# Kernel optimization log

Hardware: AMD Instinct MI355X
Metric: run time of the kernel (lower is better)

## Reference

```python
import jax, jax.numpy as jnp
import numpy as np
from jax import lax

B, DIM, DIM_OUT, NH = 8, 512, 512, 8
HD = DIM_OUT // NH          # 64, also the depthwise-conv channel count
SQ, SKV = (1, 1), (2, 2)    # stride_q, stride_kv
PAD = 1                      # kernel 3 -> padding 3//2
SCALE = HD ** -0.5
EPS = 1e-6


def _dw_conv(x, w, stride):
    # x: [N, C, H, W], w: [C, 1, kh, kw]; depthwise conv (groups = C), no bias
    return lax.conv_general_dilated(
        x, w, window_strides=stride, padding=[(PAD, PAD), (PAD, PAD)],
        dimension_numbers=('NCHW', 'OIHW', 'NCHW'),
        feature_group_count=x.shape[1])


def _ln(x, w, b):
    m = jnp.mean(x, -1, keepdims=True)
    v = jnp.var(x, -1, keepdims=True)
    return (x - m) * lax.rsqrt(v + EPS) * w + b


def _pool(t, w, stride, ln_w, ln_b, H, W):
    # t: [B, NH, 1+H*W, HD] with cls token at index 0
    Bn = t.shape[0]
    cls = t[:, :, :1, :]
    body = t[:, :, 1:, :].reshape(Bn * NH, H, W, HD).transpose(0, 3, 1, 2)
    body = _dw_conv(body, w, stride)
    ph, pw = body.shape[2], body.shape[3]
    body = body.reshape(Bn, NH, HD, ph * pw).transpose(0, 1, 3, 2)
    out = jnp.concatenate([cls, body], axis=2)
    return _ln(out, ln_w, ln_b), (ph, pw)


def _rel_bias(r_q4, q_shape, k_shape, rel_pos_h, rel_pos_w):
    # r_q4: [B, NH, q_h*q_w, HD] (cls token stripped)
    q_h, q_w = q_shape
    k_h, k_w = k_shape

    def dist(qs, ks):
        qr, kr = max(ks / qs, 1.0), max(qs / ks, 1.0)
        d = np.arange(qs)[:, None] * qr - np.arange(ks)[None, :] * kr + (ks - 1) * kr
        return d.astype(np.int64)

    Rh = rel_pos_h[dist(q_h, k_h)]  # [q_h, k_h, HD]
    Rw = rel_pos_w[dist(q_w, k_w)]  # [q_w, k_w, HD]
    r_q = r_q4.reshape(r_q4.shape[0], NH, q_h, q_w, HD)
    rel_h = jnp.einsum('byhwc,hkc->byhwk', r_q, Rh)  # [B,NH,q_h,q_w,k_h]
    rel_w = jnp.einsum('byhwc,wkc->byhwk', r_q, Rw)  # [B,NH,q_h,q_w,k_w]
    return rel_h[..., :, None] + rel_w[..., None, :]  # [B,NH,q_h,q_w,k_h,k_w]


def setup_inputs() -> dict:
    key = jax.random.key(0)
    ks = jax.random.split(key, 16)
    H = W = 56
    N = H * W + 1
    rel_dim = 2 * H - 1  # 111
    return {
        'x': jax.random.normal(ks[0], (B, N, DIM), jnp.float32),
        'qkv_w': jax.random.normal(ks[1], (3 * DIM_OUT, DIM), jnp.float32) * DIM ** -0.5,
        'qkv_b': jax.random.normal(ks[2], (3 * DIM_OUT,), jnp.float32) * 0.02,
        'proj_w': jax.random.normal(ks[3], (DIM_OUT, DIM_OUT), jnp.float32) * DIM_OUT ** -0.5,
        'proj_b': jax.random.normal(ks[4], (DIM_OUT,), jnp.float32) * 0.02,
        'pool_q_w': jax.random.normal(ks[5], (HD, 1, 3, 3), jnp.float32) / 3.0,
        'pool_k_w': jax.random.normal(ks[6], (HD, 1, 3, 3), jnp.float32) / 3.0,
        'pool_v_w': jax.random.normal(ks[7], (HD, 1, 3, 3), jnp.float32) / 3.0,
        'lnq_w': 1.0 + 0.1 * jax.random.normal(ks[8], (HD,), jnp.float32),
        'lnq_b': 0.02 * jax.random.normal(ks[9], (HD,), jnp.float32),
        'lnk_w': 1.0 + 0.1 * jax.random.normal(ks[10], (HD,), jnp.float32),
        'lnk_b': 0.02 * jax.random.normal(ks[11], (HD,), jnp.float32),
        'lnv_w': 1.0 + 0.1 * jax.random.normal(ks[12], (HD,), jnp.float32),
        'lnv_b': 0.02 * jax.random.normal(ks[13], (HD,), jnp.float32),
        'rel_pos_h': 0.02 * jax.random.normal(ks[14], (rel_dim, HD), jnp.float32),
        'rel_pos_w': 0.02 * jax.random.normal(ks[15], (rel_dim, HD), jnp.float32),
        'hw_h': 56,
        'hw_w': 56,
    }


def reference(x, qkv_w, qkv_b, proj_w, proj_b, pool_q_w, pool_k_w, pool_v_w,
              lnq_w, lnq_b, lnk_w, lnk_b, lnv_w, lnv_b, rel_pos_h, rel_pos_w,
              hw_h, hw_w):
    Bn, N, _ = x.shape
    qkv = (x @ qkv_w.T + qkv_b).reshape(Bn, N, 3, NH, HD).transpose(2, 0, 3, 1, 4)
    q, k, v = qkv[0], qkv[1], qkv[2]  # each [B, NH, N, HD]
    q, q_shape = _pool(q, pool_q_w, SQ, lnq_w, lnq_b, hw_h, hw_w)
    k, k_shape = _pool(k, pool_k_w, SKV, lnk_w, lnk_b, hw_h, hw_w)
    v, _ = _pool(v, pool_v_w, SKV, lnv_w, lnv_b, hw_h, hw_w)
    attn = (q * SCALE) @ k.swapaxes(-2, -1)  # [B, NH, Nq, Nk]
    q_h, q_w = q_shape
    k_h, k_w = k_shape
    bias = _rel_bias(q[:, :, 1:, :], q_shape, k_shape, rel_pos_h, rel_pos_w)
    blk = attn[:, :, 1:, 1:].reshape(Bn, NH, q_h, q_w, k_h, k_w) + bias
    attn = attn.at[:, :, 1:, 1:].set(blk.reshape(Bn, NH, q_h * q_w, k_h * k_w))
    attn = jax.nn.softmax(attn, axis=-1)
    out = attn @ v                                   # [B, NH, Nq, HD]
    out = out.at[:, :, 1:, :].add(q[:, :, 1:, :])    # residual on non-cls rows
    out = out.transpose(0, 2, 1, 3).reshape(Bn, -1, DIM_OUT)
    return out @ proj_w.T + proj_b
```

## Files before the change

### kernel.cpp

```cpp
#include <hip/hip_runtime.h>
#include <hip/hip_bf16.h>
#include <cstdint>
#include <cstddef>

#define BB 8
#define NHH 8
#define NQ 3137
#define NKV 785
#define HDIM 64
#define MROWS (BB*NQ)
#define SCALE 0.125f
#define VTP 832

typedef unsigned short ushort_t;
typedef __attribute__((ext_vector_type(8))) short s16x8;
typedef __attribute__((ext_vector_type(4))) float f32x4;
typedef __attribute__((ext_vector_type(16))) float f32x16;

__device__ __forceinline__ float bf2f(ushort_t u) {
  union { unsigned int i; float f; } v; v.i = ((unsigned int)u) << 16; return v.f;
}
__device__ __forceinline__ ushort_t f2bf(float f) {
  union { float f; unsigned int i; } v; v.f = f;
  unsigned int r = v.i + 0x7fffu + ((v.i >> 16) & 1u);
  return (ushort_t)(r >> 16);
}
__device__ __forceinline__ unsigned int cvt_pk_bf16(float lo, float hi) {
  unsigned int r;
  asm("v_cvt_pk_bf16_f32 %0, %1, %2" : "=v"(r) : "v"(lo), "v"(hi));
  return r;
}
__device__ __forceinline__ s16x8 lds_frag(const ushort_t* base, int row, int slot) {
  const char* p = (const char*)base + row * 128 + (((slot ^ (row & 7)) & 7) << 4);
  return *(const s16x8*)p;
}

__global__ __launch_bounds__(256) void cast_bf16_kernel(
    const float* __restrict__ in, ushort_t* __restrict__ outp, int n4) {
  const int i = blockIdx.x * 256 + threadIdx.x;
  if (i >= n4) return;
  const float4 v = ((const float4*)in)[i];
  ushort_t o[4] = { f2bf(v.x), f2bf(v.y), f2bf(v.z), f2bf(v.w) };
  *(uint2*)(outp + (size_t)i * 4) = *(const uint2*)o;
}

template<int EPI>
__global__ __launch_bounds__(256) void mfma_gemm_bt(
    const ushort_t* __restrict__ A, const ushort_t* __restrict__ W,
    const float* __restrict__ bias, void* __restrict__ outp, int M) {
  __shared__ ushort_t As[128][40];
  __shared__ ushort_t Bs[128][40];
  const int tid = threadIdx.x;
  const int l = tid & 63, w = tid >> 6;
  const int wr = w >> 1, wc = w & 1;
  const int lrow = l & 15, lk = l >> 4;
  const int m0 = blockIdx.y * 128, n0 = blockIdx.x * 128;
  const int srow = tid >> 2, sch = tid & 3;
  const int mA0 = m0 + srow      < M ? m0 + srow      : M - 1;
  const int mA1 = m0 + 64 + srow < M ? m0 + 64 + srow : M - 1;
  const size_t ar0 = (size_t)mA0 * 512, ar1 = (size_t)mA1 * 512;
  const size_t br0 = (size_t)(n0 + srow) * 512, br1 = (size_t)(n0 + 64 + srow) * 512;
  f32x4 acc[4][4];
  #pragma unroll
  for (int i = 0; i < 4; ++i) {
    #pragma unroll
    for (int j = 0; j < 4; ++j) acc[i][j] = (f32x4){0.f, 0.f, 0.f, 0.f};
  }
  for (int k0 = 0; k0 < 512; k0 += 32) {
    const uint4 a0 = *(const uint4*)(A + ar0 + k0 + sch * 8);
    const uint4 a1 = *(const uint4*)(A + ar1 + k0 + sch * 8);
    const uint4 b0 = *(const uint4*)(W + br0 + k0 + sch * 8);
    const uint4 b1 = *(const uint4*)(W + br1 + k0 + sch * 8);
    __syncthreads();
    *(uint4*)(&As[srow][sch * 8])      = a0;
    *(uint4*)(&As[64 + srow][sch * 8]) = a1;
    *(uint4*)(&Bs[srow][sch * 8])      = b0;
    *(uint4*)(&Bs[64 + srow][sch * 8]) = b1;
    __syncthreads();
    s16x8 af[4], bfr[4];
    #pragma unroll
    for (int mi = 0; mi < 4; ++mi)
      af[mi] = *(const s16x8*)(&As[wr * 64 + mi * 16 + lrow][lk * 8]);
    #pragma unroll
    for (int ni = 0; ni < 4; ++ni)
      bfr[ni] = *(const s16x8*)(&Bs[wc * 64 + ni * 16 + lrow][lk * 8]);
    #pragma unroll
    for (int mi = 0; mi < 4; ++mi) {
      #pragma unroll
      for (int ni = 0; ni < 4; ++ni)
        acc[mi][ni] = __builtin_amdgcn_mfma_f32_16x16x32_bf16(
            af[mi], bfr[ni], acc[mi][ni], 0, 0, 0);
    }
  }
  #pragma unroll
  for (int mi = 0; mi < 4; ++mi) {
    #pragma unroll
    for (int r = 0; r < 4; ++r) {
      const int m = m0 + wr * 64 + mi * 16 + 4 * lk + r;
      if (m >= M) continue;
      #pragma unroll
      for (int ni = 0; ni < 4; ++ni) {
        const int n = n0 + wc * 64 + ni * 16 + lrow;
        const float v = acc[mi][ni][r] + bias[n];
        if (EPI == 0) {
          const int which = n >> 9, y = (n >> 6) & 7, c = n & 63;
          const int b_ = m / NQ, tok = m - b_ * NQ;
          ((ushort_t*)outp)[((((size_t)which * BB + b_) * NHH + y) * NQ + tok) * HDIM + c] = f2bf(v);
        } else {
          ((float*)outp)[(size_t)m * 512 + n] = v;
        }
      }
    }
  }
}

__global__ __launch_bounds__(256) void pool_ln_kernel(
    const ushort_t* __restrict__ in, ushort_t* __restrict__ outp,
    const float* __restrict__ cw, const float* __restrict__ lnw,
    const float* __restrict__ lnb, int stride, int OW, int R) {
  const int tid = threadIdx.x;
  const int c = tid & 63;
  const int rid = blockIdx.x * 4 + (tid >> 6);
  const int by = rid / R;
  const int n = rid - by * R;
  const ushort_t* ibase = in + (size_t)by * NQ * HDIM;
  float val;
  if (n == 0) {
    val = bf2f(ibase[c]);
  } else {
    const int p = n - 1;
    const int ho = p / OW, wo = p - ho * OW;
    float s = 0.f;
    #pragma unroll
    for (int dh = 0; dh < 3; ++dh) {
      const int hh = ho * stride + dh - 1;
      if (hh < 0 || hh >= 56) continue;
      #pragma unroll
      for (int dw = 0; dw < 3; ++dw) {
        const int ww = wo * stride + dw - 1;
        if (ww < 0 || ww >= 56) continue;
        s += cw[c * 9 + dh * 3 + dw] * bf2f(ibase[(size_t)(1 + hh * 56 + ww) * HDIM + c]);
      }
    }
    val = s;
  }
  float sum = val, sq = val * val;
  #pragma unroll
  for (int off = 32; off > 0; off >>= 1) {
    sum += __shfl_xor(sum, off);
    sq  += __shfl_xor(sq,  off);
  }
  const float mean = sum * (1.f / 64.f);
  const float var  = sq * (1.f / 64.f) - mean * mean;
  const float rs = rsqrtf(var + 1e-6f);
  outp[(size_t)rid * HDIM + c] = f2bf((val - mean) * rs * lnw[c] + lnb[c]);
}

__global__ __launch_bounds__(256) void transpose_v_kernel(
    const ushort_t* __restrict__ vin, ushort_t* __restrict__ vtout) {
  __shared__ ushort_t T[64][65];
  const int tid = threadIdx.x;
  const int by = blockIdx.y;
  const int n0 = blockIdx.x * 64;
  #pragma unroll
  for (int half = 0; half < 2; ++half) {
    const int idx = tid + half * 256;
    const int r = idx >> 3, s = idx & 7;
    const int n = n0 + r;
    uint4 d = make_uint4(0u, 0u, 0u, 0u);
    if (n < NKV) d = *(const uint4*)(vin + ((size_t)by * NKV + n) * HDIM + s * 8);
    const ushort_t* dp = (const ushort_t*)&d;
    #pragma unroll
    for (int e = 0; e < 8; ++e) T[r][s * 8 + e] = dp[e];
  }
  __syncthreads();
  #pragma unroll
  for (int half = 0; half < 2; ++half) {
    const int idx = tid + half * 256;
    const int c = idx >> 3, g = idx & 7;
    ushort_t pk[8];
    #pragma unroll
    for (int e = 0; e < 8; ++e) pk[e] = T[g * 8 + e][c];
    *(uint4*)(vtout + ((size_t)by * 64 + c) * VTP + n0 + g * 8) = *(const uint4*)pk;
  }
}

__global__ __launch_bounds__(256) void relbias_mfma_kernel(
    const ushort_t* __restrict__ qb, const float* __restrict__ rph,
    const float* __restrict__ rpw, float* __restrict__ relh,
    float* __restrict__ relw) {
  const int tid = threadIdx.x;
  const int l = tid & 63, w = tid >> 6;
  const int lrow = l & 15, lk = l >> 4;
  const int hw = blockIdx.y;
  const int mode = blockIdx.z;
  const int r0 = blockIdx.x * 256 + w * 64;
  const float* tab = mode ? rpw : rph;
  float* outp = mode ? relw : relh;
  s16x8 bfr[2][2];
  #pragma unroll
  for (int ni = 0; ni < 2; ++ni) {
    const int kh = ni * 16 + lrow;
    int trow = hw - 2 * kh + 54;
    if (trow < 0) trow = 0;
    const float* tr = tab + (size_t)trow * 64 + lk * 8;
    #pragma unroll
    for (int k0 = 0; k0 < 2; ++k0) {
      const float4 t0 = *(const float4*)(tr + k0 * 32);
      const float4 t1 = *(const float4*)(tr + k0 * 32 + 4);
      s16x8 bb;
      bb[0] = (short)f2bf(t0.x); bb[1] = (short)f2bf(t0.y);
      bb[2] = (short)f2bf(t0.z); bb[3] = (short)f2bf(t0.w);
      bb[4] = (short)f2bf(t1.x); bb[5] = (short)f2bf(t1.y);
      bb[6] = (short)f2bf(t1.z); bb[7] = (short)f2bf(t1.w);
      bfr[ni][k0] = bb;
    }
  }
  s16x8 af[4][2];
  #pragma unroll
  for (int mi = 0; mi < 4; ++mi) {
    const int rA = r0 + mi * 16 + lrow;
    const int by = rA / 56, oth = rA - 56 * by;
    const int tok = mode ? (1 + oth * 56 + hw) : (1 + hw * 56 + oth);
    const ushort_t* qp = qb + ((size_t)by * NQ + tok) * HDIM + lk * 8;
    af[mi][0] = *(const s16x8*)(qp);
    af[mi][1] = *(const s16x8*)(qp + 32);
  }
  f32x4 acc[4][2];
  #pragma unroll
  for (int mi = 0; mi < 4; ++mi) {
    #pragma unroll
    for (int ni = 0; ni < 2; ++ni) acc[mi][ni] = (f32x4){0.f, 0.f, 0.f, 0.f};
  }
  #pragma unroll
  for (int k0 = 0; k0 < 2; ++k0) {
    #pragma unroll
    for (int mi = 0; mi < 4; ++mi) {
      #pragma unroll
      for (int ni = 0; ni < 2; ++ni)
        acc[mi][ni] = __builtin_amdgcn_mfma_f32_16x16x32_bf16(
            af[mi][k0], bfr[ni][k0], acc[mi][ni], 0, 0, 0);
    }
  }
  #pragma unroll
  for (int mi = 0; mi < 4; ++mi) {
    #pragma unroll
    for (int r = 0; r < 4; ++r) {
      const int row = r0 + mi * 16 + 4 * lk + r;
      const int by = row / 56, oth = row - 56 * by;
      const int p = mode ? (oth * 56 + hw) : (hw * 56 + oth);
      float* orow = outp + ((size_t)by * 3136 + p) * 28;
      #pragma unroll
      for (int ni = 0; ni < 2; ++ni) {
        const int kh = ni * 16 + lrow;
        if (kh < 28) orow[kh] = acc[mi][ni][r];
      }
    }
  }
}

__global__ __launch_bounds__(256) void attn_mfma32_kernel(
    const ushort_t* __restrict__ qb, const ushort_t* __restrict__ kb,
    const ushort_t* __restrict__ vt, const float* __restrict__ relh,
    const float* __restrict__ relw, ushort_t* __restrict__ outp) {
  __shared__ ushort_t Kl[64 * 64];
  __shared__ ushort_t Vl[64 * 64];
  __shared__ float RHl[128][29];
  __shared__ float RWl[128][29];
  const int tid = threadIdx.x;
  const int l = tid & 63, w = tid >> 6;
  const int h = l >> 5, q5 = l & 31;
  const int by = blockIdx.y;
  const int qt0 = blockIdx.x * 128;
  const int qloc = w * 32 + q5;
  const int qglob = qt0 + qloc;
  const int qcl = qglob < NQ ? qglob : NQ - 1;
  for (int i = tid; i < 128 * 28; i += 256) {
    const int r = i / 28, c = i - 28 * r;
    const int n = qt0 + r;
    float vh = 0.f, vw = 0.f;
    if (n >= 1 && n < NQ) {
      const size_t bofs = ((size_t)by * 3136 + (n - 1)) * 28 + c;
      vh = relh[bofs]; vw = relw[bofs];
    }
    RHl[r][c] = vh; RWl[r][c] = vw;
  }
  const ushort_t* qrow = qb + ((size_t)by * NQ + qcl) * HDIM;
  s16x8 qf[4];
  #pragma unroll
  for (int cb = 0; cb < 4; ++cb)
    qf[cb] = *(const s16x8*)(qrow + cb * 16 + h * 8);
  f32x16 ot0, ot1;
  #pragma unroll
  for (int i = 0; i < 16; ++i) { ot0[i] = 0.f; ot1[i] = 0.f; }
  float mr = -1e30f, lr = 0.f;
  const int srow = tid >> 3, sslot = tid & 7;
  #pragma unroll 1
  for (int it = 0; it < 13; ++it) {
    const int j0 = it * 64;
    int jA = j0 + srow;      if (jA > NKV - 1) jA = NKV - 1;
    int jB = j0 + 32 + srow; if (jB > NKV - 1) jB = NKV - 1;
    const uint4 kd0 = *(const uint4*)(kb + ((size_t)by * NKV + jA) * HDIM + sslot * 8);
    const uint4 kd1 = *(const uint4*)(kb + ((size_t)by * NKV + jB) * HDIM + sslot * 8);
    const uint4 vd0 = *(const uint4*)(vt + ((size_t)by * 64 + srow) * VTP + j0 + sslot * 8);
    const uint4 vd1 = *(const uint4*)(vt + ((size_t)by * 64 + srow + 32) * VTP + j0 + sslot * 8);
    __syncthreads();
    *(uint4*)((char*)Kl + srow * 128 + (((sslot ^ (srow & 7)) & 7) << 4)) = kd0;
    *(uint4*)((char*)Kl + (srow + 32) * 128 + (((sslot ^ ((srow + 32) & 7)) & 7) << 4)) = kd1;
    *(uint4*)((char*)Vl + srow * 128 + (((sslot ^ (srow & 7)) & 7) << 4)) = vd0;
    *(uint4*)((char*)Vl + (srow + 32) * 128 + (((sslot ^ ((srow + 32) & 7)) & 7) << 4)) = vd1;
    __syncthreads();
    f32x16 st0, st1;
    #pragma unroll
    for (int i = 0; i < 16; ++i) { st0[i] = 0.f; st1[i] = 0.f; }
    #pragma unroll
    for (int cb = 0; cb < 4; ++cb) {
      st0 = __builtin_amdgcn_mfma_f32_32x32x16_bf16(
          lds_frag(Kl, q5, cb * 2 + h), qf[cb], st0, 0, 0, 0);
      st1 = __builtin_amdgcn_mfma_f32_32x32x16_bf16(
          lds_frag(Kl, 32 + q5, cb * 2 + h), qf[cb], st1, 0, 0, 0);
    }
    float pa[16], pb[16];
    auto sval = [&](float (&pv)[16], const f32x16& st, int kt) {
      const int jbase = j0 + kt * 32 + 4 * h;
      int jc0 = jbase - 1; if (jc0 < 0) jc0 = 0;
      int khlo = jc0 / 28; if (khlo > 27) khlo = 27;
      const int khhi = khlo < 27 ? khlo + 1 : 27;
      const float rh_lo = RHl[qloc][khlo];
      const float rh_hi = RHl[qloc][khhi];
      const int jswitch = (khlo + 1) * 28 + 1;
      #pragma unroll
      for (int r = 0; r < 16; ++r) {
        const int klocal = (r & 3) + 8 * (r >> 2) + 4 * h;
        const int j = j0 + kt * 32 + klocal;
        const bool valid = j < NKV;
        const bool hasb = (j >= 1) && valid;
        const bool hi = (j >= jswitch);
        const float rhv = hi ? rh_hi : rh_lo;
        const int khv = hi ? khhi : khlo;
        int jc = j - 1; if (jc < 0) jc = 0;
        int kw = jc - 28 * khv;
        if (kw > 27) kw = 27; if (kw < 0) kw = 0;
        const float rwv = RWl[qloc][kw];
        const float sv = st[r] * SCALE + (hasb ? (rhv + rwv) : 0.f);
        pv[r] = valid ? sv : -1e30f;
      }
    };
    sval(pa, st0, 0);
    sval(pb, st1, 1);
    float mloc = pa[0];
    #pragma unroll
    for (int r = 1; r < 16; ++r) mloc = fmaxf(mloc, pa[r]);
    #pragma unroll
    for (int r = 0; r < 16; ++r) mloc = fmaxf(mloc, pb[r]);
    mloc = fmaxf(mloc, __shfl_xor(mloc, 32));
    const float mn = fmaxf(mr, mloc);
    const float sc = __expf(mr - mn);
    mr = mn;
    float ps = 0.f;
    #pragma unroll
    for (int r = 0; r < 16; ++r) { pa[r] = __expf(pa[r] - mn); ps += pa[r]; }
    #pragma unroll
    for (int r = 0; r < 16; ++r) { pb[r] = __expf(pb[r] - mn); ps += pb[r]; }
    ps += __shfl_xor(ps, 32);
    lr = lr * sc + ps;
    #pragma unroll
    for (int i = 0; i < 16; ++i) { ot0[i] *= sc; ot1[i] *= sc; }
    auto pvstep = [&](const float (&pv)[16], int kt) {
      #pragma unroll
      for (int kbk = 0; kbk < 2; ++kbk) {
        const unsigned int pk01 = cvt_pk_bf16(pv[kbk * 8 + 0], pv[kbk * 8 + 1]);
        const unsigned int pk23 = cvt_pk_bf16(pv[kbk * 8 + 2], pv[kbk * 8 + 3]);
        const unsigned int pk45 = cvt_pk_bf16(pv[kbk * 8 + 4], pv[kbk * 8 + 5]);
        const unsigned int pk67 = cvt_pk_bf16(pv[kbk * 8 + 6], pv[kbk * 8 + 7]);
        const unsigned int sA = (unsigned int)__shfl_xor((int)pk01, 32);
        const unsigned int sB = (unsigned int)__shfl_xor((int)pk45, 32);
        const unsigned int sC = (unsigned int)__shfl_xor((int)pk23, 32);
        const unsigned int sD = (unsigned int)__shfl_xor((int)pk67, 32);
        int4 fw;
        fw.x = (int)(h ? sB : pk01);
        fw.y = (int)(h ? sD : pk23);
        fw.z = (int)(h ? pk45 : sA);
        fw.w = (int)(h ? pk67 : sC);
        s16x8 pf;
        __builtin_memcpy(&pf, &fw, 16);
        const int slot = kt * 4 + kbk * 2 + h;
        ot0 = __builtin_amdgcn_mfma_f32_32x32x16_bf16(
            lds_frag(Vl, q5, slot), pf, ot0, 0, 0, 0);
        ot1 = __builtin_amdgcn_mfma_f32_32x32x16_bf16(
            lds_frag(Vl, 32 + q5, slot), pf, ot1, 0, 0, 0);
      }
    };
    pvstep(pa, 0);
    pvstep(pb, 1);
  }
  const float inv = 1.f / lr;
  if (qglob < NQ) {
    const int b_ = by >> 3, y_ = by & 7;
    ushort_t* obase = outp + ((size_t)b_ * NQ + qglob) * 512 + (size_t)y_ * 64;
    const ushort_t* rbase = qb + ((size_t)by * NQ + qglob) * HDIM;
    #pragma unroll
    for (int ch = 0; ch < 2; ++ch) {
      #pragma unroll
      for (int rg = 0; rg < 4; ++rg) {
        const int c0 = ch * 32 + 8 * rg + 4 * h;
        float vv[4];
        #pragma unroll
        for (int e = 0; e < 4; ++e)
          vv[e] = (ch ? ot1[rg * 4 + e] : ot0[rg * 4 + e]) * inv;
        if (qglob > 0) {
          #pragma unroll
          for (int e = 0; e < 4; ++e) vv[e] += bf2f(rbase[c0 + e]);
        }
        ushort_t pk[4] = { f2bf(vv[0]), f2bf(vv[1]), f2bf(vv[2]), f2bf(vv[3]) };
        *(uint2*)(obase + c0) = *(const uint2*)pk;
      }
    }
  }
}

extern "C" void kernel_launch(void* const* d_in, const int* in_sizes, int n_in,
                              void* d_out, int out_size, void* d_ws, size_t ws_size,
                              hipStream_t stream) {
  const float* x        = (const float*)d_in[0];
  const float* qkv_w    = (const float*)d_in[1];
  const float* qkv_b    = (const float*)d_in[2];
  const float* proj_w   = (const float*)d_in[3];
  const float* proj_b   = (const float*)d_in[4];
  const float* pool_q_w = (const float*)d_in[5];
  const float* pool_k_w = (const float*)d_in[6];
  const float* pool_v_w = (const float*)d_in[7];
  const float* lnq_w    = (const float*)d_in[8];
  const float* lnq_b    = (const float*)d_in[9];
  const float* lnk_w    = (const float*)d_in[10];
  const float* lnk_b    = (const float*)d_in[11];
  const float* lnv_w    = (const float*)d_in[12];
  const float* lnv_b    = (const float*)d_in[13];
  const float* rel_pos_h = (const float*)d_in[14];
  const float* rel_pos_w = (const float*)d_in[15];

  constexpr size_t E1 = (size_t)BB * NHH * NQ * HDIM;
  constexpr size_t EKV = (size_t)BB * NHH * NKV * HDIM;
  char* ws = (char*)d_ws;
  size_t off = 0;
  ushort_t* x_bf     = (ushort_t*)(ws + off); off += (size_t)MROWS * 512 * 2;
  ushort_t* qkvw_bf  = (ushort_t*)(ws + off); off += (size_t)1536 * 512 * 2;
  ushort_t* projw_bf = (ushort_t*)(ws + off); off += (size_t)512 * 512 * 2;
  ushort_t* qkv_raw  = (ushort_t*)(ws + off); off += 3 * E1 * 2;
  ushort_t* q_bf     = (ushort_t*)(ws + off); off += E1 * 2;
  ushort_t* k_bf     = (ushort_t*)(ws + off); off += EKV * 2;
  ushort_t* v_bf     = (ushort_t*)(ws + off); off += EKV * 2;
  ushort_t* v_t      = (ushort_t*)(ws + off); off += (size_t)64 * 64 * VTP * 2;
  float*    rel_h    = (float*)(ws + off);    off += (size_t)64 * 3136 * 28 * 4;
  float*    rel_w    = (float*)(ws + off);    off += (size_t)64 * 3136 * 28 * 4;
  ushort_t* attn_bf  = qkv_raw;

  cast_bf16_kernel<<<(MROWS * 512 / 4 + 255) / 256, 256, 0, stream>>>(x, x_bf, MROWS * 512 / 4);
  cast_bf16_kernel<<<768, 256, 0, stream>>>(qkv_w, qkvw_bf, 1536 * 512 / 4);
  cast_bf16_kernel<<<256, 256, 0, stream>>>(proj_w, projw_bf, 512 * 512 / 4);

  mfma_gemm_bt<0><<<dim3(12, 197), 256, 0, stream>>>(x_bf, qkvw_bf, qkv_b, (void*)qkv_raw, MROWS);

  pool_ln_kernel<<<(64 * NQ) / 4,  256, 0, stream>>>(qkv_raw,          q_bf, pool_q_w, lnq_w, lnq_b, 1, 56, NQ);
  pool_ln_kernel<<<(64 * NKV) / 4, 256, 0, stream>>>(qkv_raw + E1,     k_bf, pool_k_w, lnk_w, lnk_b, 2, 28, NKV);
  pool_ln_kernel<<<(64 * NKV) / 4, 256, 0, stream>>>(qkv_raw + 2 * E1, v_bf, pool_v_w, lnv_w, lnv_b, 2, 28, NKV);

  transpose_v_kernel<<<dim3(13, 64), 256, 0, stream>>>(v_bf, v_t);

  relbias_mfma_kernel<<<dim3(14, 56, 2), 256, 0, stream>>>(q_bf, rel_pos_h, rel_pos_w, rel_h, rel_w);

  attn_mfma32_kernel<<<dim3(25, 64), 256, 0, stream>>>(q_bf, k_bf, v_t, rel_h, rel_w, attn_bf);

  mfma_gemm_bt<1><<<dim3(4, 197), 256, 0, stream>>>(attn_bf, projw_bf, proj_b, d_out, MROWS);
}
```

Before: 479.4 us.

## Fold relative-position bias into augmented QK dot product and fuse bf16 casts into GEMMs

Q and K are widened to 128 channels. Q carries the scaled values plus the rel-h and rel-w bias terms, and K carries one-hot indicator columns for its row and column index, so the QK MFMA produces score plus bias directly. This removes the fp32 rel_h/rel_w buffers, the LDS staging of those tables and the per-element bias gather in the attention loop. Separately, the fp32-to-bf16 cast kernels are dropped and the conversion happens on load inside the GEMM. The cost is twice the QK MFMA work and twice the K LDS footprint, and the scale and bias are now rounded to bf16 before the dot product.

```diff
diff --git a/kernel.cpp b/kernel.cpp
--- a/kernel.cpp
+++ b/kernel.cpp
@@ -8,6 +8,7 @@
 #define NQ 3137
 #define NKV 785
 #define HDIM 64
+#define AUG 128
 #define MROWS (BB*NQ)
 #define SCALE 0.125f
 #define VTP 832
@@ -30,23 +31,18 @@
   asm("v_cvt_pk_bf16_f32 %0, %1, %2" : "=v"(r) : "v"(lo), "v"(hi));
   return r;
 }
-__device__ __forceinline__ s16x8 lds_frag(const ushort_t* base, int row, int slot) {
+__device__ __forceinline__ s16x8 lds_frag8(const ushort_t* base, int row, int slot) {
   const char* p = (const char*)base + row * 128 + (((slot ^ (row & 7)) & 7) << 4);
   return *(const s16x8*)p;
 }
-
-__global__ __launch_bounds__(256) void cast_bf16_kernel(
-    const float* __restrict__ in, ushort_t* __restrict__ outp, int n4) {
-  const int i = blockIdx.x * 256 + threadIdx.x;
-  if (i >= n4) return;
-  const float4 v = ((const float4*)in)[i];
-  ushort_t o[4] = { f2bf(v.x), f2bf(v.y), f2bf(v.z), f2bf(v.w) };
-  *(uint2*)(outp + (size_t)i * 4) = *(const uint2*)o;
-}
-
-template<int EPI>
+__device__ __forceinline__ s16x8 lds_frag16(const ushort_t* base, int row, int slot) {
+  const char* p = (const char*)base + row * 256 + (((slot ^ (row & 15)) & 15) << 4);
+  return *(const s16x8*)p;
+}
+
+template<int EPI, bool AF32, bool WF32>
 __global__ __launch_bounds__(256) void mfma_gemm_bt(
-    const ushort_t* __restrict__ A, const ushort_t* __restrict__ W,
+    const void* __restrict__ Ap, const void* __restrict__ Wp,
     const float* __restrict__ bias, void* __restrict__ outp, int M) {
   __shared__ ushort_t As[128][40];
   __shared__ ushort_t Bs[128][40];
@@ -60,6 +56,19 @@
   const int mA1 = m0 + 64 + srow < M ? m0 + 64 + srow : M - 1;
   const size_t ar0 = (size_t)mA0 * 512, ar1 = (size_t)mA1 * 512;
   const size_t br0 = (size_t)(n0 + srow) * 512, br1 = (size_t)(n0 + 64 + srow) * 512;
+  const ushort_t* Ab = (const ushort_t*)Ap;
+  const float*    Af = (const float*)Ap;
+  const ushort_t* Wb = (const ushort_t*)Wp;
+  const float*    Wf = (const float*)Wp;
+  auto ld8 = [&](const ushort_t* pb, const float* pf, size_t ofs, bool f32) -> uint4 {
+    if (!f32) return *(const uint4*)(pb + ofs);
+    const float4 v0 = *(const float4*)(pf + ofs);
+    const float4 v1 = *(const float4*)(pf + ofs + 4);
+    uint4 r;
+    r.x = cvt_pk_bf16(v0.x, v0.y); r.y = cvt_pk_bf16(v0.z, v0.w);
+    r.z = cvt_pk_bf16(v1.x, v1.y); r.w = cvt_pk_bf16(v1.z, v1.w);
+    return r;
+  };
   f32x4 acc[4][4];
   #pragma unroll
   for (int i = 0; i < 4; ++i) {
@@ -67,10 +76,10 @@
     for (int j = 0; j < 4; ++j) acc[i][j] = (f32x4){0.f, 0.f, 0.f, 0.f};
   }
   for (int k0 = 0; k0 < 512; k0 += 32) {
-    const uint4 a0 = *(const uint4*)(A + ar0 + k0 + sch * 8);
-    const uint4 a1 = *(const uint4*)(A + ar1 + k0 + sch * 8);
-    const uint4 b0 = *(const uint4*)(W + br0 + k0 + sch * 8);
-    const uint4 b1 = *(const uint4*)(W + br1 + k0 + sch * 8);
+    const uint4 a0 = ld8(Ab, Af, ar0 + k0 + sch * 8, AF32);
+    const uint4 a1 = ld8(Ab, Af, ar1 + k0 + sch * 8, AF32);
+    const uint4 b0 = ld8(Wb, Wf, br0 + k0 + sch * 8, WF32);
+    const uint4 b1 = ld8(Wb, Wf, br1 + k0 + sch * 8, WF32);
     __syncthreads();
     *(uint4*)(&As[srow][sch * 8])      = a0;
     *(uint4*)(&As[64 + srow][sch * 8]) = a1;
@@ -114,8 +123,10 @@
   }
 }
 
+template<int MODE>
 __global__ __launch_bounds__(256) void pool_ln_kernel(
-    const ushort_t* __restrict__ in, ushort_t* __restrict__ outp,
+    const ushort_t* __restrict__ in, ushort_t* __restrict__ out0,
+    ushort_t* __restrict__ out1,
     const float* __restrict__ cw, const float* __restrict__ lnw,
     const float* __restrict__ lnb, int stride, int OW, int R) {
   const int tid = threadIdx.x;
@@ -153,7 +164,24 @@
   const float mean = sum * (1.f / 64.f);
   const float var  = sq * (1.f / 64.f) - mean * mean;
   const float rs = rsqrtf(var + 1e-6f);
-  outp[(size_t)rid * HDIM + c] = f2bf((val - mean) * rs * lnw[c] + lnb[c]);
+  const float lno = (val - mean) * rs * lnw[c] + lnb[c];
+  if (MODE == 0) {
+    out0[(size_t)rid * HDIM + c] = f2bf(lno);
+  } else if (MODE == 1) {
+    out0[(size_t)rid * HDIM + c] = f2bf(lno);
+    out1[(size_t)rid * AUG + c] = f2bf(lno * SCALE);
+    out1[(size_t)rid * AUG + 64 + c] = 0;
+  } else {
+    out0[(size_t)rid * AUG + c] = f2bf(lno);
+    ushort_t aug = 0;
+    if (n >= 1) {
+      const int p = n - 1;
+      const int kh = p / 28, kw = p - 28 * kh;
+      if (c < 28) { if (c == kh) aug = 0x3F80; }
+      else if (c < 56) { if (c - 28 == kw) aug = 0x3F80; }
+    }
+    out0[(size_t)rid * AUG + 64 + c] = aug;
+  }
 }
 
 __global__ __launch_bounds__(256) void transpose_v_kernel(
@@ -187,8 +215,7 @@
 
 __global__ __launch_bounds__(256) void relbias_mfma_kernel(
     const ushort_t* __restrict__ qb, const float* __restrict__ rph,
-    const float* __restrict__ rpw, float* __restrict__ relh,
-    float* __restrict__ relw) {
+    const float* __restrict__ rpw, ushort_t* __restrict__ qaug) {
   const int tid = threadIdx.x;
   const int l = tid & 63, w = tid >> 6;
   const int lrow = l & 15, lk = l >> 4;
@@ -196,7 +223,6 @@
   const int mode = blockIdx.z;
   const int r0 = blockIdx.x * 256 + w * 64;
   const float* tab = mode ? rpw : rph;
-  float* outp = mode ? relw : relh;
   s16x8 bfr[2][2];
   #pragma unroll
   for (int ni = 0; ni < 2; ++ni) {
@@ -242,31 +268,30 @@
             af[mi][k0], bfr[ni][k0], acc[mi][ni], 0, 0, 0);
     }
   }
+  const int augofs = 64 + mode * 28;
   #pragma unroll
   for (int mi = 0; mi < 4; ++mi) {
     #pragma unroll
     for (int r = 0; r < 4; ++r) {
       const int row = r0 + mi * 16 + 4 * lk + r;
       const int by = row / 56, oth = row - 56 * by;
-      const int p = mode ? (oth * 56 + hw) : (hw * 56 + oth);
-      float* orow = outp + ((size_t)by * 3136 + p) * 28;
+      const int tok = 1 + (mode ? (oth * 56 + hw) : (hw * 56 + oth));
+      ushort_t* orow = qaug + ((size_t)by * NQ + tok) * AUG + augofs;
       #pragma unroll
       for (int ni = 0; ni < 2; ++ni) {
         const int kh = ni * 16 + lrow;
-        if (kh < 28) orow[kh] = acc[mi][ni][r];
+        if (kh < 28) orow[kh] = f2bf(acc[mi][ni][r]);
       }
     }
   }
 }
 
 __global__ __launch_bounds__(256) void attn_mfma32_kernel(
-    const ushort_t* __restrict__ qb, const ushort_t* __restrict__ kb,
-    const ushort_t* __restrict__ vt, const float* __restrict__ relh,
-    const float* __restrict__ relw, ushort_t* __restrict__ outp) {
-  __shared__ ushort_t Kl[64 * 64];
+    const ushort_t* __restrict__ qaug, const ushort_t* __restrict__ kaug,
+    const ushort_t* __restrict__ qb, const ushort_t* __restrict__ vt,
+    ushort_t* __restrict__ outp) {
+  __shared__ ushort_t Kl[64 * AUG];
   __shared__ ushort_t Vl[64 * 64];
-  __shared__ float RHl[128][29];
-  __shared__ float RWl[128][29];
   const int tid = threadIdx.x;
   const int l = tid & 63, w = tid >> 6;
   const int h = l >> 5, q5 = l & 31;
@@ -275,79 +300,62 @@
   const int qloc = w * 32 + q5;
   const int qglob = qt0 + qloc;
   const int qcl = qglob < NQ ? qglob : NQ - 1;
-  for (int i = tid; i < 128 * 28; i += 256) {
-    const int r = i / 28, c = i - 28 * r;
-    const int n = qt0 + r;
-    float vh = 0.f, vw = 0.f;
-    if (n >= 1 && n < NQ) {
-      const size_t bofs = ((size_t)by * 3136 + (n - 1)) * 28 + c;
-      vh = relh[bofs]; vw = relw[bofs];
-    }
-    RHl[r][c] = vh; RWl[r][c] = vw;
-  }
-  const ushort_t* qrow = qb + ((size_t)by * NQ + qcl) * HDIM;
-  s16x8 qf[4];
-  #pragma unroll
-  for (int cb = 0; cb < 4; ++cb)
+  const ushort_t* qrow = qaug + ((size_t)by * NQ + qcl) * AUG;
+  s16x8 qf[8];
+  #pragma unroll
+  for (int cb = 0; cb < 8; ++cb)
     qf[cb] = *(const s16x8*)(qrow + cb * 16 + h * 8);
   f32x16 ot0, ot1;
   #pragma unroll
   for (int i = 0; i < 16; ++i) { ot0[i] = 0.f; ot1[i] = 0.f; }
   float mr = -1e30f, lr = 0.f;
-  const int srow = tid >> 3, sslot = tid & 7;
+  const int krow = tid >> 2, ks4 = (tid & 3) * 4;
+  const int vrow = tid >> 3, vslot = tid & 7;
+  int jK = krow; if (jK > NKV - 1) jK = NKV - 1;
   #pragma unroll 1
   for (int it = 0; it < 13; ++it) {
     const int j0 = it * 64;
-    int jA = j0 + srow;      if (jA > NKV - 1) jA = NKV - 1;
-    int jB = j0 + 32 + srow; if (jB > NKV - 1) jB = NKV - 1;
-    const uint4 kd0 = *(const uint4*)(kb + ((size_t)by * NKV + jA) * HDIM + sslot * 8);
-    const uint4 kd1 = *(const uint4*)(kb + ((size_t)by * NKV + jB) * HDIM + sslot * 8);
-    const uint4 vd0 = *(const uint4*)(vt + ((size_t)by * 64 + srow) * VTP + j0 + sslot * 8);
-    const uint4 vd1 = *(const uint4*)(vt + ((size_t)by * 64 + srow + 32) * VTP + j0 + sslot * 8);
+    jK = j0 + krow; if (jK > NKV - 1) jK = NKV - 1;
+    const ushort_t* ksrc = kaug + ((size_t)by * NKV + jK) * AUG + ks4 * 8;
+    const uint4 kd0 = *(const uint4*)(ksrc);
+    const uint4 kd1 = *(const uint4*)(ksrc + 8);
+    const uint4 kd2 = *(const uint4*)(ksrc + 16);
+    const uint4 kd3 = *(const uint4*)(ksrc + 24);
+    const uint4 vd0 = *(const uint4*)(vt + ((size_t)by * 64 + vrow) * VTP + j0 + vslot * 8);
+    const uint4 vd1 = *(const uint4*)(vt + ((size_t)by * 64 + vrow + 32) * VTP + j0 + vslot * 8);
     __syncthreads();
-    *(uint4*)((char*)Kl + srow * 128 + (((sslot ^ (srow & 7)) & 7) << 4)) = kd0;
-    *(uint4*)((char*)Kl + (srow + 32) * 128 + (((sslot ^ ((srow + 32) & 7)) & 7) << 4)) = kd1;
-    *(uint4*)((char*)Vl + srow * 128 + (((sslot ^ (srow & 7)) & 7) << 4)) = vd0;
-    *(uint4*)((char*)Vl + (srow + 32) * 128 + (((sslot ^ ((srow + 32) & 7)) & 7) << 4)) = vd1;
+    {
+      char* kbase = (char*)Kl + krow * 256;
+      const int rm = krow & 15;
+      *(uint4*)(kbase + (((ks4 + 0) ^ rm) << 4)) = kd0;
+      *(uint4*)(kbase + (((ks4 + 1) ^ rm) << 4)) = kd1;
+      *(uint4*)(kbase + (((ks4 + 2) ^ rm) << 4)) = kd2;
+      *(uint4*)(kbase + (((ks4 + 3) ^ rm) << 4)) = kd3;
+      *(uint4*)((char*)Vl + vrow * 128 + (((vslot ^ (vrow & 7)) & 7) << 4)) = vd0;
+      *(uint4*)((char*)Vl + (vrow + 32) * 128 + (((vslot ^ ((vrow + 32) & 7)) & 7) << 4)) = vd1;
+    }
     __syncthreads();
     f32x16 st0, st1;
     #pragma unroll
     for (int i = 0; i < 16; ++i) { st0[i] = 0.f; st1[i] = 0.f; }
     #pragma unroll
-    for (int cb = 0; cb < 4; ++cb) {
+    for (int cb = 0; cb < 8; ++cb) {
       st0 = __builtin_amdgcn_mfma_f32_32x32x16_bf16(
-          lds_frag(Kl, q5, cb * 2 + h), qf[cb], st0, 0, 0, 0);
+          lds_frag16(Kl, q5, cb * 2 + h), qf[cb], st0, 0, 0, 0);
       st1 = __builtin_amdgcn_mfma_f32_32x32x16_bf16(
-          lds_frag(Kl, 32 + q5, cb * 2 + h), qf[cb], st1, 0, 0, 0);
+          lds_frag16(Kl, 32 + q5, cb * 2 + h), qf[cb], st1, 0, 0, 0);
     }
     float pa[16], pb[16];
-    auto sval = [&](float (&pv)[16], const f32x16& st, int kt) {
-      const int jbase = j0 + kt * 32 + 4 * h;
-      int jc0 = jbase - 1; if (jc0 < 0) jc0 = 0;
-      int khlo = jc0 / 28; if (khlo > 27) khlo = 27;
-      const int khhi = khlo < 27 ? khlo + 1 : 27;
-      const float rh_lo = RHl[qloc][khlo];
-      const float rh_hi = RHl[qloc][khhi];
-      const int jswitch = (khlo + 1) * 28 + 1;
+    #pragma unroll
+    for (int r = 0; r < 16; ++r) { pa[r] = st0[r]; pb[r] = st1[r]; }
+    if (it == 12) {
       #pragma unroll
       for (int r = 0; r < 16; ++r) {
         const int klocal = (r & 3) + 8 * (r >> 2) + 4 * h;
-        const int j = j0 + kt * 32 + klocal;
-        const bool valid = j < NKV;
-        const bool hasb = (j >= 1) && valid;
-        const bool hi = (j >= jswitch);
-        const float rhv = hi ? rh_hi : rh_lo;
-        const int khv = hi ? khhi : khlo;
-        int jc = j - 1; if (jc < 0) jc = 0;
-        int kw = jc - 28 * khv;
-        if (kw > 27) kw = 27; if (kw < 0) kw = 0;
-        const float rwv = RWl[qloc][kw];
-        const float sv = st[r] * SCALE + (hasb ? (rhv + rwv) : 0.f);
-        pv[r] = valid ? sv : -1e30f;
-      }
-    };
-    sval(pa, st0, 0);
-    sval(pb, st1, 1);
+        if (768 + klocal >= NKV) pa[r] = -1e30f;
+        pb[r] = -1e30f;
+      }
+    }
     float mloc = pa[0];
     #pragma unroll
     for (int r = 1; r < 16; ++r) mloc = fmaxf(mloc, pa[r]);
@@ -386,9 +394,9 @@
         __builtin_memcpy(&pf, &fw, 16);
         const int slot = kt * 4 + kbk * 2 + h;
         ot0 = __builtin_amdgcn_mfma_f32_32x32x16_bf16(
-            lds_frag(Vl, q5, slot), pf, ot0, 0, 0, 0);
+            lds_frag8(Vl, q5, slot), pf, ot0, 0, 0, 0);
         ot1 = __builtin_amdgcn_mfma_f32_32x32x16_bf16(
-            lds_frag(Vl, 32 + q5, slot), pf, ot1, 0, 0, 0);
+            lds_frag8(Vl, 32 + q5, slot), pf, ot1, 0, 0, 0);
       }
     };
     pvstep(pa, 0);
@@ -440,36 +448,29 @@
   const float* rel_pos_w = (const float*)d_in[15];
 
   constexpr size_t E1 = (size_t)BB * NHH * NQ * HDIM;
-  constexpr size_t EKV = (size_t)BB * NHH * NKV * HDIM;
   char* ws = (char*)d_ws;
   size_t off = 0;
-  ushort_t* x_bf     = (ushort_t*)(ws + off); off += (size_t)MROWS * 512 * 2;
-  ushort_t* qkvw_bf  = (ushort_t*)(ws + off); off += (size_t)1536 * 512 * 2;
-  ushort_t* projw_bf = (ushort_t*)(ws + off); off += (size_t)512 * 512 * 2;
-  ushort_t* qkv_raw  = (ushort_t*)(ws + off); off += 3 * E1 * 2;
-  ushort_t* q_bf     = (ushort_t*)(ws + off); off += E1 * 2;
-  ushort_t* k_bf     = (ushort_t*)(ws + off); off += EKV * 2;
-  ushort_t* v_bf     = (ushort_t*)(ws + off); off += EKV * 2;
-  ushort_t* v_t      = (ushort_t*)(ws + off); off += (size_t)64 * 64 * VTP * 2;
-  float*    rel_h    = (float*)(ws + off);    off += (size_t)64 * 3136 * 28 * 4;
-  float*    rel_w    = (float*)(ws + off);    off += (size_t)64 * 3136 * 28 * 4;
-  ushort_t* attn_bf  = qkv_raw;
-
-  cast_bf16_kernel<<<(MROWS * 512 / 4 + 255) / 256, 256, 0, stream>>>(x, x_bf, MROWS * 512 / 4);
-  cast_bf16_kernel<<<768, 256, 0, stream>>>(qkv_w, qkvw_bf, 1536 * 512 / 4);
-  cast_bf16_kernel<<<256, 256, 0, stream>>>(proj_w, projw_bf, 512 * 512 / 4);
-
-  mfma_gemm_bt<0><<<dim3(12, 197), 256, 0, stream>>>(x_bf, qkvw_bf, qkv_b, (void*)qkv_raw, MROWS);
-
-  pool_ln_kernel<<<(64 * NQ) / 4,  256, 0, stream>>>(qkv_raw,          q_bf, pool_q_w, lnq_w, lnq_b, 1, 56, NQ);
-  pool_ln_kernel<<<(64 * NKV) / 4, 256, 0, stream>>>(qkv_raw + E1,     k_bf, pool_k_w, lnk_w, lnk_b, 2, 28, NKV);
-  pool_ln_kernel<<<(64 * NKV) / 4, 256, 0, stream>>>(qkv_raw + 2 * E1, v_bf, pool_v_w, lnv_w, lnv_b, 2, 28, NKV);
+  ushort_t* qkv_raw = (ushort_t*)(ws + off); off += 3 * E1 * 2;
+  ushort_t* q_bf    = (ushort_t*)(ws + off); off += E1 * 2;
+  ushort_t* qaug    = (ushort_t*)(ws + off); off += (size_t)BB * NHH * NQ * AUG * 2;
+  ushort_t* kaug    = (ushort_t*)(ws + off); off += (size_t)BB * NHH * NKV * AUG * 2;
+  ushort_t* v_bf    = (ushort_t*)(ws + off); off += (size_t)BB * NHH * NKV * HDIM * 2;
+  ushort_t* v_t     = (ushort_t*)(ws + off); off += (size_t)64 * 64 * VTP * 2;
+  ushort_t* attn_bf = qkv_raw;
+
+  mfma_gemm_bt<0, true, true><<<dim3(12, 197), 256, 0, stream>>>(
+      x, qkv_w, qkv_b, (void*)qkv_raw, MROWS);
+
+  pool_ln_kernel<1><<<(64 * NQ) / 4,  256, 0, stream>>>(qkv_raw,          q_bf, qaug, pool_q_w, lnq_w, lnq_b, 1, 56, NQ);
+  pool_ln_kernel<2><<<(64 * NKV) / 4, 256, 0, stream>>>(qkv_raw + E1,     kaug, nullptr, pool_k_w, lnk_w, lnk_b, 2, 28, NKV);
+  pool_ln_kernel<0><<<(64 * NKV) / 4, 256, 0, stream>>>(qkv_raw + 2 * E1, v_bf, nullptr, pool_v_w, lnv_w, lnv_b, 2, 28, NKV);
 
   transpose_v_kernel<<<dim3(13, 64), 256, 0, stream>>>(v_bf, v_t);
 
-  relbias_mfma_kernel<<<dim3(14, 56, 2), 256, 0, stream>>>(q_bf, rel_pos_h, rel_pos_w, rel_h, rel_w);
-
-  attn_mfma32_kernel<<<dim3(25, 64), 256, 0, stream>>>(q_bf, k_bf, v_t, rel_h, rel_w, attn_bf);
-
-  mfma_gemm_bt<1><<<dim3(4, 197), 256, 0, stream>>>(attn_bf, projw_bf, proj_b, d_out, MROWS);
-}
+  relbias_mfma_kernel<<<dim3(14, 56, 2), 256, 0, stream>>>(q_bf, rel_pos_h, rel_pos_w, qaug);
+
+  attn_mfma32_kernel<<<dim3(25, 64), 256, 0, stream>>>(qaug, kaug, q_bf, v_t, attn_bf);
+
+  mfma_gemm_bt<1, false, true><<<dim3(4, 197), 256, 0, stream>>>(
+      attn_bf, proj_w, proj_b, d_out, MROWS);
+}
```

New measurement: 472.6 us. No clear change (-1.4%).
